# Kernel tuning notes

Hardware: AMD Instinct MI355X
Metric: run time of the kernel (lower is better)

## Reference

```python
import jax, jax.numpy as jnp
import numpy as np

DIM = 768
HEADS = 12
HEAD_DIM = DIM // HEADS
HIDDEN = int(DIM * 4.0)
EPS = 1e-5


def _layernorm(x, g, b):
    mu = jnp.mean(x, axis=-1, keepdims=True)
    var = jnp.mean(jnp.square(x - mu), axis=-1, keepdims=True)
    return (x - mu) * jax.lax.rsqrt(var + EPS) * g + b


def setup_inputs() -> dict:
    key = jax.random.key(0)
    ks = jax.random.split(key, 8)
    s_in = 1.0 / np.sqrt(DIM)
    s_hid = 1.0 / np.sqrt(HIDDEN)
    return {
        "x": jax.random.normal(ks[0], (2, 2048, DIM), dtype=jnp.float32),
        "ln1_g": jnp.ones((DIM,), jnp.float32),
        "ln1_b": jnp.zeros((DIM,), jnp.float32),
        "w_qkv": jax.random.normal(ks[1], (DIM, 3 * DIM), jnp.float32) * s_in,
        "w_proj": jax.random.normal(ks[2], (DIM, DIM), jnp.float32) * s_in,
        "b_proj": jnp.zeros((DIM,), jnp.float32),
        "ln2_g": jnp.ones((DIM,), jnp.float32),
        "ln2_b": jnp.zeros((DIM,), jnp.float32),
        "w_fc1": jax.random.normal(ks[3], (DIM, HIDDEN), jnp.float32) * s_in,
        "b_fc1": jnp.zeros((HIDDEN,), jnp.float32),
        "w_fc2": jax.random.normal(ks[4], (HIDDEN, DIM), jnp.float32) * s_hid,
        "b_fc2": jnp.zeros((DIM,), jnp.float32),
    }


def reference(x, ln1_g, ln1_b, w_qkv, w_proj, b_proj, ln2_g, ln2_b, w_fc1, b_fc1, w_fc2, b_fc2):
    b, n, c = x.shape
    scale = HEAD_DIM ** -0.5

    # --- attention branch ---
    h = _layernorm(x, ln1_g, ln1_b)
    qkv = (h @ w_qkv).reshape(b, n, 3, HEADS, HEAD_DIM)
    q, k, v = jnp.moveaxis(qkv, 2, 0)          # each [b, n, H, hd]
    attn = jnp.einsum("bqhd,bkhd->bhqk", q, k) * scale
    attn = jax.nn.softmax(attn, axis=-1)       # [b, H, n, n] (naive, materialized)
    o = jnp.einsum("bhqk,bkhd->bqhd", attn, v).reshape(b, n, c)
    x = x + o @ w_proj + b_proj

    # --- MLP branch ---
    h2 = _layernorm(x, ln2_g, ln2_b)
    m = jax.nn.gelu(h2 @ w_fc1 + b_fc1, approximate=False)
    x = x + m @ w_fc2 + b_fc2
    return x
```

## Files before the change

### kernel.cpp

```cpp
#include <hip/hip_runtime.h>
#include <math.h>


typedef unsigned short u16;
typedef __attribute__((ext_vector_type(8))) short short8;
typedef __attribute__((ext_vector_type(4))) float f32x4;

#define TOKENS 4096
#define DIM    768
#define QKV_N  2304
#define HID    3072
#define NSEQ   2048
#define NHEAD  12
#define HDIM   64

__device__ __forceinline__ float bf2f(u16 u) {
  union { unsigned i; float f; } v; v.i = ((unsigned)u) << 16; return v.f;
}
__device__ __forceinline__ u16 f2bf(float f) {
  union { float f; unsigned i; } v; v.f = f;
  unsigned r = v.i + 0x7fffu + ((v.i >> 16) & 1u);
  return (u16)(r >> 16);
}
__device__ __forceinline__ u16 f2bf_trunc(float f) {
  union { float f; unsigned i; } v; v.f = f;
  return (u16)(v.i >> 16);
}

__device__ __forceinline__ void async_copy16(const u16* g, u16* l) {
  __builtin_amdgcn_global_load_lds(
      (const __attribute__((address_space(1))) unsigned int*)(unsigned long long)g,
      (__attribute__((address_space(3))) unsigned int*)(unsigned int)(unsigned long long)l,
      16, 0, 0);
}

__global__ __launch_bounds__(256) void transpose_k(const float* __restrict__ in,
                                                   u16* __restrict__ out,
                                                   int R, int C) {
  __shared__ u16 t[32][33];
  int c0 = blockIdx.x * 32, r0 = blockIdx.y * 32;
  int tx = threadIdx.x, ty = threadIdx.y;
#pragma unroll
  for (int i = 0; i < 4; i++)
    t[ty + i * 8][tx] = f2bf(in[(size_t)(r0 + ty + i * 8) * C + c0 + tx]);
  __syncthreads();
#pragma unroll
  for (int i = 0; i < 4; i++)
    out[(size_t)(c0 + ty + i * 8) * R + r0 + tx] = t[tx][ty + i * 8];
}

__global__ __launch_bounds__(256) void transpose_v(const u16* __restrict__ qkv,
                                                   u16* __restrict__ vt) {
  __shared__ u16 t[32][33];
  int c0 = blockIdx.x * 32;
  int r0 = blockIdx.y * 32;
  int tx = threadIdx.x, ty = threadIdx.y;
#pragma unroll
  for (int i = 0; i < 4; i++)
    t[ty + i * 8][tx] = qkv[(size_t)(r0 + ty + i * 8) * QKV_N + 2 * DIM + c0 + tx];
  __syncthreads();
  int b = r0 >> 11, tok = (r0 & 2047) + tx;
#pragma unroll
  for (int i = 0; i < 4; i++)
    vt[((size_t)b * DIM + c0 + ty + i * 8) * NSEQ + tok] = t[tx][ty + i * 8];
}

template <bool INF32>
__global__ __launch_bounds__(256) void ln_kernel(const void* __restrict__ xin,
                                                 const float* __restrict__ g,
                                                 const float* __restrict__ b,
                                                 u16* __restrict__ out) {
  int wave = threadIdx.x >> 6, lane = threadIdx.x & 63;
  int token = blockIdx.x * 4 + wave;
  float v[12];
  if (INF32) {
    const float4* xr = (const float4*)((const float*)xin + (size_t)token * DIM);
#pragma unroll
    for (int w = 0; w < 3; w++) {
      float4 q = xr[lane + w * 64];
      v[w * 4 + 0] = q.x; v[w * 4 + 1] = q.y; v[w * 4 + 2] = q.z; v[w * 4 + 3] = q.w;
    }
  } else {
    const ushort4* xr = (const ushort4*)((const u16*)xin + (size_t)token * DIM);
#pragma unroll
    for (int w = 0; w < 3; w++) {
      ushort4 q = xr[lane + w * 64];
      v[w * 4 + 0] = bf2f(q.x); v[w * 4 + 1] = bf2f(q.y);
      v[w * 4 + 2] = bf2f(q.z); v[w * 4 + 3] = bf2f(q.w);
    }
  }
  float s = 0.f;
#pragma unroll
  for (int i = 0; i < 12; i++) s += v[i];
#pragma unroll
  for (int off = 32; off > 0; off >>= 1) s += __shfl_xor(s, off);
  float mu = s * (1.0f / DIM);
  float ss = 0.f;
#pragma unroll
  for (int i = 0; i < 12; i++) { float d = v[i] - mu; ss += d * d; }
#pragma unroll
  for (int off = 32; off > 0; off >>= 1) ss += __shfl_xor(ss, off);
  float rs = rsqrtf(ss * (1.0f / DIM) + 1e-5f);

  ushort4* orow = (ushort4*)(out + (size_t)token * DIM);
  const float4* g4 = (const float4*)g;
  const float4* b4 = (const float4*)b;
#pragma unroll
  for (int w = 0; w < 3; w++) {
    float4 gq = g4[lane + w * 64], bq = b4[lane + w * 64];
    ushort4 o;
    o.x = f2bf((v[w * 4 + 0] - mu) * rs * gq.x + bq.x);
    o.y = f2bf((v[w * 4 + 1] - mu) * rs * gq.y + bq.y);
    o.z = f2bf((v[w * 4 + 2] - mu) * rs * gq.z + bq.z);
    o.w = f2bf((v[w * 4 + 3] - mu) * rs * gq.w + bq.w);
    orow[lane + w * 64] = o;
  }
}

template <int BM, int BN, int EPI>
__global__ __launch_bounds__(256, 3) void gemm_bt(
    const u16* __restrict__ A, const u16* __restrict__ BT,
    void* __restrict__ Cout, const float* __restrict__ bias,
    const void* __restrict__ resid, int M, int N, int K) {
  constexpr int MT = BM / 32, NT = BN / 32;
  constexpr int ACH = BM / 16;
  constexpr int CPW = (BM + BN) / 64;
  __shared__ __align__(16) u16 Alds[2][BM * 32];
  __shared__ __align__(16) u16 Blds[2][BN * 32];
  const int tid = threadIdx.x;
  const int lane = tid & 63, wave = tid >> 6;
  const int wr = wave >> 1, wc = wave & 1;
  const int bm = blockIdx.y * BM, bn = blockIdx.x * BN;
  const int c16 = lane & 15, quad = lane >> 4;
  const int l4 = lane >> 2, lc = (lane & 3) * 8;

  f32x4 acc[MT][NT];
#pragma unroll
  for (int i = 0; i < MT; i++)
#pragma unroll
    for (int j = 0; j < NT; j++) acc[i][j] = (f32x4){0.f, 0.f, 0.f, 0.f};

  const u16* gsrc[CPW];
  u16* ldst[CPW];
  int hstep[CPW];
#pragma unroll
  for (int c = 0; c < CPW; c++) {
    int chunk = wave * CPW + c;
    if (chunk < ACH) {
      gsrc[c] = A + (size_t)(bm + chunk * 16 + l4) * K + lc;
      ldst[c] = Alds[0] + chunk * 512;
      hstep[c] = BM * 32;
    } else {
      int bc = chunk - ACH;
      gsrc[c] = BT + (size_t)(bn + bc * 16 + l4) * K + lc;
      ldst[c] = Blds[0] + bc * 512;
      hstep[c] = BN * 32;
    }
  }

  for (int kk = 0; kk < K; kk += 64) {
    __syncthreads();
#pragma unroll
    for (int c = 0; c < CPW; c++) {
      async_copy16(gsrc[c] + kk, ldst[c]);
      async_copy16(gsrc[c] + kk + 32, ldst[c] + hstep[c]);
    }
    __syncthreads();
#pragma unroll
    for (int ks = 0; ks < 2; ks++) {
      short8 af[MT], bfr[NT];
#pragma unroll
      for (int mt = 0; mt < MT; mt++)
        af[mt] = *(const short8*)(Alds[ks] + (wr * (BM / 2) + mt * 16 + c16) * 32 + quad * 8);
#pragma unroll
      for (int nt = 0; nt < NT; nt++)
        bfr[nt] = *(const short8*)(Blds[ks] + (wc * (BN / 2) + nt * 16 + c16) * 32 + quad * 8);
#pragma unroll
      for (int mt = 0; mt < MT; mt++)
#pragma unroll
        for (int nt = 0; nt < NT; nt++)
          acc[mt][nt] = __builtin_amdgcn_mfma_f32_16x16x32_bf16(af[mt], bfr[nt],
                                                                acc[mt][nt], 0, 0, 0);
    }
  }

#pragma unroll
  for (int mt = 0; mt < MT; mt++) {
#pragma unroll
    for (int nt = 0; nt < NT; nt++) {
      int col = bn + wc * (BN / 2) + nt * 16 + c16;
      float bv = (EPI != 0) ? bias[col] : 0.f;
#pragma unroll
      for (int r = 0; r < 4; r++) {
        int row = bm + wr * (BM / 2) + mt * 16 + quad * 4 + r;
        float vv = acc[mt][nt][r];
        if (EPI == 1) {
          vv += bv + ((const float*)resid)[(size_t)row * N + col];
          ((u16*)Cout)[(size_t)row * N + col] = f2bf(vv);
        } else if (EPI == 2) {
          vv += bv;
          vv = 0.5f * vv * (1.0f + erff(vv * 0.70710678118654752f));
          ((u16*)Cout)[(size_t)row * N + col] = f2bf(vv);
        } else if (EPI == 3) {
          vv += bv + bf2f(((const u16*)resid)[(size_t)row * N + col]);
          ((float*)Cout)[(size_t)row * N + col] = vv;
        } else {
          ((u16*)Cout)[(size_t)row * N + col] = f2bf(vv);
        }
      }
    }
  }
}

__global__ __launch_bounds__(256) void attn_kernel(const u16* __restrict__ qkv,
                                                   const u16* __restrict__ vt,
                                                   u16* __restrict__ o) {
  const int tid = threadIdx.x;
  const int lane = tid & 63, wave = tid >> 6;
  const int c16 = lane & 15, quad = lane >> 4;
  const int qt = blockIdx.x & 31;
  const int bh = blockIdx.x >> 5;
  const int bb = bh / NHEAD, h = bh % NHEAD;
  __shared__ __align__(16) u16 Klds[64 * 64];
  __shared__ __align__(16) u16 Vtlds[64 * 64];
  __shared__ __align__(16) u16 Plds[4][16 * 64];
  const size_t base = (size_t)bb * NSEQ * QKV_N;
  const int q0 = qt * 64 + wave * 16;

  const u16* qp = qkv + base + (size_t)(q0 + c16) * QKV_N + h * HDIM;
  short8 qf0 = *(const short8*)(qp + quad * 8);
  short8 qf1 = *(const short8*)(qp + 32 + quad * 8);

  float Ls[4] = {0.f, 0.f, 0.f, 0.f};
  f32x4 Of[4];
#pragma unroll
  for (int dt = 0; dt < 4; dt++) Of[dt] = (f32x4){0.f, 0.f, 0.f, 0.f};

  const int lr = lane >> 3;
  const int swz = ((lane & 7) ^ lr) * 8;
  const int row0 = wave * 16 + lr;
  const u16* kbase = qkv + base + (size_t)row0 * QKV_N + DIM + h * HDIM + (lane & 7) * 8;
  const u16* vbase = vt + ((size_t)bh * HDIM + row0) * NSEQ + (lane & 7) * 8;
  const int cswz0 = (quad ^ (c16 & 7)) * 8;
  const int cswz1 = ((quad + 4) ^ (c16 & 7)) * 8;
  const float SC = 0.18033688011112042f;

  for (int kt = 0; kt < NSEQ; kt += 64) {
    uint4 k0 = *(const uint4*)(kbase + (size_t)kt * QKV_N);
    uint4 k1 = *(const uint4*)(kbase + (size_t)(kt + 8) * QKV_N);
    uint4 v0 = *(const uint4*)(vbase + kt);
    uint4 v1 = *(const uint4*)(vbase + 8 * NSEQ + kt);
    __syncthreads();
    *(uint4*)(Klds + row0 * 64 + swz) = k0;
    *(uint4*)(Klds + (row0 + 8) * 64 + swz) = k1;
    *(uint4*)(Vtlds + row0 * 64 + swz) = v0;
    *(uint4*)(Vtlds + (row0 + 8) * 64 + swz) = v1;
    __syncthreads();

    f32x4 S[4];
#pragma unroll
    for (int nt = 0; nt < 4; nt++) {
      S[nt] = (f32x4){0.f, 0.f, 0.f, 0.f};
      const u16* krow = Klds + (nt * 16 + c16) * 64;
      short8 ka = *(const short8*)(krow + cswz0);
      short8 kb = *(const short8*)(krow + cswz1);
      S[nt] = __builtin_amdgcn_mfma_f32_16x16x32_bf16(qf0, ka, S[nt], 0, 0, 0);
      S[nt] = __builtin_amdgcn_mfma_f32_16x16x32_bf16(qf1, kb, S[nt], 0, 0, 0);
    }

    u16* pl = Plds[wave];
    const int el = c16 & 7, ch = c16 >> 3;
#pragma unroll
    for (int r = 0; r < 4; r++) {
      float p0 = __builtin_amdgcn_exp2f(S[0][r] * SC);
      float p1 = __builtin_amdgcn_exp2f(S[1][r] * SC);
      float p2 = __builtin_amdgcn_exp2f(S[2][r] * SC);
      float p3 = __builtin_amdgcn_exp2f(S[3][r] * SC);
      Ls[r] += (p0 + p1) + (p2 + p3);
      u16* pr = pl + (quad * 4 + r) * 64;
      const int r7 = (quad * 4 + r) & 7;
      pr[((0 + ch) ^ r7) * 8 + el] = f2bf_trunc(p0);
      pr[((2 + ch) ^ r7) * 8 + el] = f2bf_trunc(p1);
      pr[((4 + ch) ^ r7) * 8 + el] = f2bf_trunc(p2);
      pr[((6 + ch) ^ r7) * 8 + el] = f2bf_trunc(p3);
    }

    short8 pf0 = *(const short8*)(pl + c16 * 64 + cswz0);
    short8 pf1 = *(const short8*)(pl + c16 * 64 + cswz1);
#pragma unroll
    for (int dt = 0; dt < 4; dt++) {
      const u16* vrow = Vtlds + (dt * 16 + c16) * 64;
      short8 va = *(const short8*)(vrow + cswz0);
      short8 vb = *(const short8*)(vrow + cswz1);
      Of[dt] = __builtin_amdgcn_mfma_f32_16x16x32_bf16(pf0, va, Of[dt], 0, 0, 0);
      Of[dt] = __builtin_amdgcn_mfma_f32_16x16x32_bf16(pf1, vb, Of[dt], 0, 0, 0);
    }
  }

#pragma unroll
  for (int r = 0; r < 4; r++) {
    float t = Ls[r];
    t += __shfl_xor(t, 1); t += __shfl_xor(t, 2);
    t += __shfl_xor(t, 4); t += __shfl_xor(t, 8);
    Ls[r] = t;
  }

#pragma unroll
  for (int dt = 0; dt < 4; dt++)
#pragma unroll
    for (int r = 0; r < 4; r++) {
      int token = q0 + quad * 4 + r;
      float val = Of[dt][r] / Ls[r];
      o[(size_t)(bb * NSEQ + token) * DIM + h * HDIM + dt * 16 + c16] = f2bf(val);
    }
}

extern "C" void kernel_launch(void* const* d_in, const int* in_sizes, int n_in,
                              void* d_out, int out_size, void* d_ws, size_t ws_size,
                              hipStream_t stream) {
  (void)in_sizes; (void)n_in; (void)out_size; (void)ws_size;
  const float* x      = (const float*)d_in[0];
  const float* ln1_g  = (const float*)d_in[1];
  const float* ln1_b  = (const float*)d_in[2];
  const float* w_qkv  = (const float*)d_in[3];
  const float* w_proj = (const float*)d_in[4];
  const float* b_proj = (const float*)d_in[5];
  const float* ln2_g  = (const float*)d_in[6];
  const float* ln2_b  = (const float*)d_in[7];
  const float* w_fc1  = (const float*)d_in[8];
  const float* b_fc1  = (const float*)d_in[9];
  const float* w_fc2  = (const float*)d_in[10];
  const float* b_fc2  = (const float*)d_in[11];
  float* out = (float*)d_out;

  char* p = (char*)d_ws;
  u16* h_bf   = (u16*)p; p += (size_t)TOKENS * DIM * 2;
  u16* qkv_bf = (u16*)p; p += (size_t)TOKENS * QKV_N * 2;
  u16* o_bf   = (u16*)p; p += (size_t)TOKENS * DIM * 2;
  u16* x1_bf  = (u16*)p; p += (size_t)TOKENS * DIM * 2;
  u16* wprojT = (u16*)p; p += (size_t)DIM * DIM * 2;
  u16* wfc1T  = (u16*)p; p += (size_t)HID * DIM * 2;
  u16* wfc2T  = (u16*)p; p += (size_t)DIM * HID * 2;
  u16* wqkvT  = (u16*)p; p += (size_t)QKV_N * DIM * 2;
  u16* vtb    = (u16*)p; p += (size_t)TOKENS * DIM * 2;
  u16* m_bf   = qkv_bf;

  dim3 tb(32, 8);
  transpose_k<<<dim3(QKV_N / 32, DIM / 32), tb, 0, stream>>>(w_qkv, wqkvT, DIM, QKV_N);
  transpose_k<<<dim3(DIM / 32, DIM / 32), tb, 0, stream>>>(w_proj, wprojT, DIM, DIM);
  transpose_k<<<dim3(HID / 32, DIM / 32), tb, 0, stream>>>(w_fc1, wfc1T, DIM, HID);
  transpose_k<<<dim3(DIM / 32, HID / 32), tb, 0, stream>>>(w_fc2, wfc2T, HID, DIM);

  ln_kernel<true><<<TOKENS / 4, 256, 0, stream>>>(x, ln1_g, ln1_b, h_bf);
  gemm_bt<128, 128, 0><<<dim3(QKV_N / 128, TOKENS / 128), 256, 0, stream>>>(
      h_bf, wqkvT, qkv_bf, nullptr, nullptr, TOKENS, QKV_N, DIM);
  transpose_v<<<dim3(DIM / 32, TOKENS / 32), tb, 0, stream>>>(qkv_bf, vtb);
  attn_kernel<<<dim3(2 * NHEAD * (NSEQ / 64)), 256, 0, stream>>>(qkv_bf, vtb, o_bf);
  gemm_bt<64, 128, 1><<<dim3(DIM / 128, TOKENS / 64), 256, 0, stream>>>(
      o_bf, wprojT, x1_bf, b_proj, x, TOKENS, DIM, DIM);
  ln_kernel<false><<<TOKENS / 4, 256, 0, stream>>>(x1_bf, ln2_g, ln2_b, h_bf);
  gemm_bt<128, 128, 2><<<dim3(HID / 128, TOKENS / 128), 256, 0, stream>>>(
      h_bf, wfc1T, m_bf, b_fc1, nullptr, TOKENS, HID, DIM);
  gemm_bt<64, 128, 3><<<dim3(DIM / 128, TOKENS / 64), 256, 0, stream>>>(
      m_bf, wfc2T, out, b_fc2, x1_bf, TOKENS, DIM, HID);
}
```

Baseline: 293.8 us.

## Give each attention wave two query tiles with 128-thread blocks; shrink QKV GEMM tile

The attention kernel now runs 2 waves per block, each handling 32 query rows (two 16-row MFMA tiles). Each K/V fragment read from LDS is reused across both tiles, halving LDS reads per MFMA, and the K/Vt tile staging is split over fewer threads with more loads each. The QKV projection GEMM also moves from 128x128 to 64x128 tiles, doubling the block count for better CU coverage. In exchange, register use per thread grows and the attention kernel has half as many waves per block to hide latency.

```diff
diff --git a/kernel.cpp b/kernel.cpp
--- a/kernel.cpp
+++ b/kernel.cpp
@@ -212,7 +212,7 @@
   }
 }
 
-__global__ __launch_bounds__(256) void attn_kernel(const u16* __restrict__ qkv,
+__global__ __launch_bounds__(128) void attn_kernel(const u16* __restrict__ qkv,
                                                    const u16* __restrict__ vt,
                                                    u16* __restrict__ o) {
   const int tid = threadIdx.x;
@@ -223,96 +223,123 @@
   const int bb = bh / NHEAD, h = bh % NHEAD;
   __shared__ __align__(16) u16 Klds[64 * 64];
   __shared__ __align__(16) u16 Vtlds[64 * 64];
-  __shared__ __align__(16) u16 Plds[4][16 * 64];
+  __shared__ __align__(16) u16 Plds[2][2][16 * 64];
   const size_t base = (size_t)bb * NSEQ * QKV_N;
-  const int q0 = qt * 64 + wave * 16;
-
-  const u16* qp = qkv + base + (size_t)(q0 + c16) * QKV_N + h * HDIM;
-  short8 qf0 = *(const short8*)(qp + quad * 8);
-  short8 qf1 = *(const short8*)(qp + 32 + quad * 8);
-
-  float Ls[4] = {0.f, 0.f, 0.f, 0.f};
-  f32x4 Of[4];
-#pragma unroll
-  for (int dt = 0; dt < 4; dt++) Of[dt] = (f32x4){0.f, 0.f, 0.f, 0.f};
-
-  const int lr = lane >> 3;
-  const int swz = ((lane & 7) ^ lr) * 8;
-  const int row0 = wave * 16 + lr;
-  const u16* kbase = qkv + base + (size_t)row0 * QKV_N + DIM + h * HDIM + (lane & 7) * 8;
-  const u16* vbase = vt + ((size_t)bh * HDIM + row0) * NSEQ + (lane & 7) * 8;
+  const int q0 = qt * 64 + wave * 32;
+
+  short8 qf[2][2];
+#pragma unroll
+  for (int mt = 0; mt < 2; mt++) {
+    const u16* qp = qkv + base + (size_t)(q0 + mt * 16 + c16) * QKV_N + h * HDIM;
+    qf[mt][0] = *(const short8*)(qp + quad * 8);
+    qf[mt][1] = *(const short8*)(qp + 32 + quad * 8);
+  }
+
+  float Ls[2][4] = {{0.f, 0.f, 0.f, 0.f}, {0.f, 0.f, 0.f, 0.f}};
+  f32x4 Of[2][4];
+#pragma unroll
+  for (int mt = 0; mt < 2; mt++)
+#pragma unroll
+    for (int dt = 0; dt < 4; dt++) Of[mt][dt] = (f32x4){0.f, 0.f, 0.f, 0.f};
+
+  const int c8 = tid & 7, trow = tid >> 3;
+  const int sw = ((c8 ^ (trow & 7)) * 8);
+  const u16* kbase = qkv + base + (size_t)trow * QKV_N + DIM + h * HDIM + c8 * 8;
+  const u16* vbase = vt + ((size_t)bh * HDIM + trow) * NSEQ + c8 * 8;
   const int cswz0 = (quad ^ (c16 & 7)) * 8;
   const int cswz1 = ((quad + 4) ^ (c16 & 7)) * 8;
   const float SC = 0.18033688011112042f;
 
   for (int kt = 0; kt < NSEQ; kt += 64) {
-    uint4 k0 = *(const uint4*)(kbase + (size_t)kt * QKV_N);
-    uint4 k1 = *(const uint4*)(kbase + (size_t)(kt + 8) * QKV_N);
-    uint4 v0 = *(const uint4*)(vbase + kt);
-    uint4 v1 = *(const uint4*)(vbase + 8 * NSEQ + kt);
+    uint4 kv[4], vv[4];
+#pragma unroll
+    for (int j = 0; j < 4; j++) {
+      kv[j] = *(const uint4*)(kbase + (size_t)(kt + 16 * j) * QKV_N);
+      vv[j] = *(const uint4*)(vbase + (size_t)(16 * j) * NSEQ + kt);
+    }
     __syncthreads();
-    *(uint4*)(Klds + row0 * 64 + swz) = k0;
-    *(uint4*)(Klds + (row0 + 8) * 64 + swz) = k1;
-    *(uint4*)(Vtlds + row0 * 64 + swz) = v0;
-    *(uint4*)(Vtlds + (row0 + 8) * 64 + swz) = v1;
+#pragma unroll
+    for (int j = 0; j < 4; j++) {
+      *(uint4*)(Klds + (trow + 16 * j) * 64 + sw) = kv[j];
+      *(uint4*)(Vtlds + (trow + 16 * j) * 64 + sw) = vv[j];
+    }
     __syncthreads();
 
-    f32x4 S[4];
+    f32x4 S[2][4];
 #pragma unroll
     for (int nt = 0; nt < 4; nt++) {
-      S[nt] = (f32x4){0.f, 0.f, 0.f, 0.f};
       const u16* krow = Klds + (nt * 16 + c16) * 64;
       short8 ka = *(const short8*)(krow + cswz0);
       short8 kb = *(const short8*)(krow + cswz1);
-      S[nt] = __builtin_amdgcn_mfma_f32_16x16x32_bf16(qf0, ka, S[nt], 0, 0, 0);
-      S[nt] = __builtin_amdgcn_mfma_f32_16x16x32_bf16(qf1, kb, S[nt], 0, 0, 0);
-    }
-
-    u16* pl = Plds[wave];
+#pragma unroll
+      for (int mt = 0; mt < 2; mt++) {
+        f32x4 s = (f32x4){0.f, 0.f, 0.f, 0.f};
+        s = __builtin_amdgcn_mfma_f32_16x16x32_bf16(qf[mt][0], ka, s, 0, 0, 0);
+        s = __builtin_amdgcn_mfma_f32_16x16x32_bf16(qf[mt][1], kb, s, 0, 0, 0);
+        S[mt][nt] = s;
+      }
+    }
+
     const int el = c16 & 7, ch = c16 >> 3;
 #pragma unroll
-    for (int r = 0; r < 4; r++) {
-      float p0 = __builtin_amdgcn_exp2f(S[0][r] * SC);
-      float p1 = __builtin_amdgcn_exp2f(S[1][r] * SC);
-      float p2 = __builtin_amdgcn_exp2f(S[2][r] * SC);
-      float p3 = __builtin_amdgcn_exp2f(S[3][r] * SC);
-      Ls[r] += (p0 + p1) + (p2 + p3);
-      u16* pr = pl + (quad * 4 + r) * 64;
-      const int r7 = (quad * 4 + r) & 7;
-      pr[((0 + ch) ^ r7) * 8 + el] = f2bf_trunc(p0);
-      pr[((2 + ch) ^ r7) * 8 + el] = f2bf_trunc(p1);
-      pr[((4 + ch) ^ r7) * 8 + el] = f2bf_trunc(p2);
-      pr[((6 + ch) ^ r7) * 8 + el] = f2bf_trunc(p3);
-    }
-
-    short8 pf0 = *(const short8*)(pl + c16 * 64 + cswz0);
-    short8 pf1 = *(const short8*)(pl + c16 * 64 + cswz1);
+    for (int mt = 0; mt < 2; mt++) {
+      u16* pl = Plds[wave][mt];
+#pragma unroll
+      for (int r = 0; r < 4; r++) {
+        float p0 = __builtin_amdgcn_exp2f(S[mt][0][r] * SC);
+        float p1 = __builtin_amdgcn_exp2f(S[mt][1][r] * SC);
+        float p2 = __builtin_amdgcn_exp2f(S[mt][2][r] * SC);
+        float p3 = __builtin_amdgcn_exp2f(S[mt][3][r] * SC);
+        Ls[mt][r] += (p0 + p1) + (p2 + p3);
+        u16* pr = pl + (quad * 4 + r) * 64;
+        const int r7 = (quad * 4 + r) & 7;
+        pr[((0 + ch) ^ r7) * 8 + el] = f2bf_trunc(p0);
+        pr[((2 + ch) ^ r7) * 8 + el] = f2bf_trunc(p1);
+        pr[((4 + ch) ^ r7) * 8 + el] = f2bf_trunc(p2);
+        pr[((6 + ch) ^ r7) * 8 + el] = f2bf_trunc(p3);
+      }
+    }
+
+    short8 pf[2][2];
+#pragma unroll
+    for (int mt = 0; mt < 2; mt++) {
+      const u16* pl = Plds[wave][mt];
+      pf[mt][0] = *(const short8*)(pl + c16 * 64 + cswz0);
+      pf[mt][1] = *(const short8*)(pl + c16 * 64 + cswz1);
+    }
 #pragma unroll
     for (int dt = 0; dt < 4; dt++) {
       const u16* vrow = Vtlds + (dt * 16 + c16) * 64;
       short8 va = *(const short8*)(vrow + cswz0);
       short8 vb = *(const short8*)(vrow + cswz1);
-      Of[dt] = __builtin_amdgcn_mfma_f32_16x16x32_bf16(pf0, va, Of[dt], 0, 0, 0);
-      Of[dt] = __builtin_amdgcn_mfma_f32_16x16x32_bf16(pf1, vb, Of[dt], 0, 0, 0);
-    }
-  }
-
-#pragma unroll
-  for (int r = 0; r < 4; r++) {
-    float t = Ls[r];
-    t += __shfl_xor(t, 1); t += __shfl_xor(t, 2);
-    t += __shfl_xor(t, 4); t += __shfl_xor(t, 8);
-    Ls[r] = t;
-  }
-
-#pragma unroll
-  for (int dt = 0; dt < 4; dt++)
+#pragma unroll
+      for (int mt = 0; mt < 2; mt++) {
+        Of[mt][dt] = __builtin_amdgcn_mfma_f32_16x16x32_bf16(pf[mt][0], va, Of[mt][dt], 0, 0, 0);
+        Of[mt][dt] = __builtin_amdgcn_mfma_f32_16x16x32_bf16(pf[mt][1], vb, Of[mt][dt], 0, 0, 0);
+      }
+    }
+  }
+
+#pragma unroll
+  for (int mt = 0; mt < 2; mt++)
 #pragma unroll
     for (int r = 0; r < 4; r++) {
-      int token = q0 + quad * 4 + r;
-      float val = Of[dt][r] / Ls[r];
-      o[(size_t)(bb * NSEQ + token) * DIM + h * HDIM + dt * 16 + c16] = f2bf(val);
-    }
+      float t = Ls[mt][r];
+      t += __shfl_xor(t, 1); t += __shfl_xor(t, 2);
+      t += __shfl_xor(t, 4); t += __shfl_xor(t, 8);
+      Ls[mt][r] = t;
+    }
+
+#pragma unroll
+  for (int mt = 0; mt < 2; mt++)
+#pragma unroll
+    for (int dt = 0; dt < 4; dt++)
+#pragma unroll
+      for (int r = 0; r < 4; r++) {
+        int token = q0 + mt * 16 + quad * 4 + r;
+        float val = Of[mt][dt][r] / Ls[mt][r];
+        o[(size_t)(bb * NSEQ + token) * DIM + h * HDIM + dt * 16 + c16] = f2bf(val);
+      }
 }
 
 extern "C" void kernel_launch(void* const* d_in, const int* in_sizes, int n_in,
@@ -352,10 +379,10 @@
   transpose_k<<<dim3(DIM / 32, HID / 32), tb, 0, stream>>>(w_fc2, wfc2T, HID, DIM);
 
   ln_kernel<true><<<TOKENS / 4, 256, 0, stream>>>(x, ln1_g, ln1_b, h_bf);
-  gemm_bt<128, 128, 0><<<dim3(QKV_N / 128, TOKENS / 128), 256, 0, stream>>>(
+  gemm_bt<64, 128, 0><<<dim3(QKV_N / 128, TOKENS / 64), 256, 0, stream>>>(
       h_bf, wqkvT, qkv_bf, nullptr, nullptr, TOKENS, QKV_N, DIM);
   transpose_v<<<dim3(DIM / 32, TOKENS / 32), tb, 0, stream>>>(qkv_bf, vtb);
-  attn_kernel<<<dim3(2 * NHEAD * (NSEQ / 64)), 256, 0, stream>>>(qkv_bf, vtb, o_bf);
+  attn_kernel<<<dim3(2 * NHEAD * (NSEQ / 64)), 128, 0, stream>>>(qkv_bf, vtb, o_bf);
   gemm_bt<64, 128, 1><<<dim3(DIM / 128, TOKENS / 64), 256, 0, stream>>>(
       o_bf, wprojT, x1_bf, b_proj, x, TOKENS, DIM, DIM);
   ln_kernel<false><<<TOKENS / 4, 256, 0, stream>>>(x1_bf, ln2_g, ln2_b, h_bf);
```

New measurement: 407.5 us. 38.7% more time.
